# Kernel tuning notes

Hardware: AMD Instinct MI355X
Metric: run time of the kernel (lower is better)

The kernel has to match this reference:

```python
import jax, jax.numpy as jnp
import numpy as np

OBS_LEN = 20
N_COORD = 2
HIDDEN = 1024  # z_dim + c_dim = 512 + 512
N = 4096


def setup_inputs() -> dict:
    key = jax.random.key(0)
    ks = jax.random.split(key, 6)
    obs_traj_rel = jax.random.normal(ks[0], (OBS_LEN, N, N_COORD), dtype=jnp.float32)
    pred_lstm_hidden = jax.random.normal(ks[1], (N, HIDDEN), dtype=jnp.float32)
    # LSTMCell params (PyTorch layout): weight_ih [4H, in], weight_hh [4H, H],
    # initialized N(0, 0.1); biases zero (per _initialize_weights).
    W_ih = 0.1 * jax.random.normal(ks[2], (4 * HIDDEN, N_COORD), dtype=jnp.float32)
    W_hh = 0.1 * jax.random.normal(ks[3], (4 * HIDDEN, HIDDEN), dtype=jnp.float32)
    b_ih = jnp.zeros((4 * HIDDEN,), dtype=jnp.float32)
    b_hh = jnp.zeros((4 * HIDDEN,), dtype=jnp.float32)
    # hidden2pos Linear: weight [n_coord, H], bias zero
    W_out = 0.1 * jax.random.normal(ks[4], (N_COORD, HIDDEN), dtype=jnp.float32)
    b_out = jnp.zeros((N_COORD,), dtype=jnp.float32)
    return {
        "obs_traj_rel": obs_traj_rel,
        "pred_lstm_hidden": pred_lstm_hidden,
        "W_ih": W_ih,
        "W_hh": W_hh,
        "b_ih": b_ih,
        "b_hh": b_hh,
        "W_out": W_out,
        "b_out": b_out,
        "variant_feats": 1,
    }


def reference(obs_traj_rel, pred_lstm_hidden, W_ih, W_hh, b_ih, b_hh, W_out, b_out, variant_feats):
    # Step 0 consumes obs[0]; step i>=1 consumes obs[i-1] (per the original loop).
    x_seq = jnp.concatenate([obs_traj_rel[:1], obs_traj_rel[:-1]], axis=0)[..., :N_COORD]
    c0 = jnp.zeros_like(pred_lstm_hidden)

    def step(carry, x_t):
        h, c = carry
        # PyTorch LSTMCell: gates = x W_ih^T + b_ih + h W_hh^T + b_hh, order i,f,g,o
        gates = x_t @ W_ih.T + b_ih + h @ W_hh.T + b_hh
        i, f, g, o = jnp.split(gates, 4, axis=-1)
        c = jax.nn.sigmoid(f) * c + jax.nn.sigmoid(i) * jnp.tanh(g)
        h = jax.nn.sigmoid(o) * jnp.tanh(c)
        out = h @ W_out.T + b_out  # [N, n_coord]
        return (h, c), out

    _, outs = jax.lax.scan(step, (pred_lstm_hidden, c0), x_seq)
    return outs  # [obs_len, N, n_coord]
```

## Files before the change

kernel.cpp:

```cpp
#include <hip/hip_runtime.h>
#include <hip/hip_bf16.h>
#include <stdint.h>

#define N_BATCH 4096
#define HID     1024
#define OBSLEN  20

#define BM  256
#define BK  64

using short8 = __attribute__((ext_vector_type(8))) short;
using f32x4  = __attribute__((ext_vector_type(4))) float;

#define AS1 __attribute__((address_space(1)))
#define AS3 __attribute__((address_space(3)))

__device__ __forceinline__ float rcpf(float x) { return __builtin_amdgcn_rcpf(x); }
__device__ __forceinline__ float sigf(float x) { return rcpf(1.f + __expf(-x)); }
__device__ __forceinline__ float tanh_(float x) {
    float a = fminf(15.f, fmaxf(-15.f, x));
    float t = __expf(-2.f * a);
    return (1.f - t) * rcpf(1.f + t);
}
__device__ __forceinline__ unsigned short f2bf(float f) {
    __hip_bfloat16 b = __float2bfloat16(f);
    return *reinterpret_cast<unsigned short*>(&b);
}
__device__ __forceinline__ float bf2f(unsigned short u) {
    unsigned int x = ((unsigned int)u) << 16;
    return __uint_as_float(x);
}

__global__ __launch_bounds__(256) void prep_kernel(
    const float4* __restrict__ Whh, const float4* __restrict__ h0,
    ushort4* __restrict__ Wg, ushort4* __restrict__ hb, float4* __restrict__ c, int n4)
{
    int i = blockIdx.x * 256 + threadIdx.x;
    if (i < n4) {
        float4 h = h0[i];
        hb[i] = make_ushort4(f2bf(h.x), f2bf(h.y), f2bf(h.z), f2bf(h.w));
        c[i] = make_float4(0.f, 0.f, 0.f, 0.f);
        int R  = i >> 8, k4 = i & 255;
        int by = R >> 8, cp = R & 255;
        int g  = (cp >> 4) & 3;
        int hl = ((cp >> 6) << 4) | (cp & 15);
        int orig = g * HID + by * 64 + hl;
        float4 w = Whh[orig * 256 + k4];
        Wg[i] = make_ushort4(f2bf(w.x), f2bf(w.y), f2bf(w.z), f2bf(w.w));
    }
}

__global__ __launch_bounds__(512, 2) void lstm_step_kernel(
    const ushort* __restrict__ hin,
    const ushort* __restrict__ Wg,
    const float*  __restrict__ xt,
    const float*  __restrict__ Wih,
    const float*  __restrict__ bih,
    const float*  __restrict__ bhh,
    float*        __restrict__ cst,
    ushort*       __restrict__ hout)
{
    __shared__ __align__(16) char lds[131072];
    const int tid  = threadIdx.x;
    const int lane = tid & 63, l15 = lane & 15, l4 = lane >> 4;
    const int wid  = tid >> 6, wr = wid >> 2, wc = wid & 3;

    const int L    = blockIdx.x + (int)gridDim.x * blockIdx.y;
    const int xcd  = L & 7, slot = L >> 3;
    const int xb   = slot & 15;
    const int yb   = (xcd << 1) | (slot >> 4);
    const int m0   = xb * BM;
    const int by   = yb;
    const int bid  = yb * 16 + xb;

    const int rowS = tid >> 3;
    const int offS = ((tid & 7) * 16) ^ ((rowS & 7) << 4);
    const ushort* aS = hin + (size_t)(m0 + rowS) * HID + (offS >> 1);
    const ushort* bS = Wg  + (size_t)(by * 256 + rowS) * HID + (offS >> 1);
    char* aD = lds + tid * 16;
    char* bD = lds + 65536 + tid * 16;

    auto stA = [&](int s, int k0, int r) {
        __builtin_amdgcn_global_load_lds(
            (const AS1 void*)(aS + k0 + (size_t)r * 64 * HID),
            (AS3 void*)(aD + s * 32768 + r * 8192), 16, 0, 0);
    };
    auto stB = [&](int s, int k0, int r) {
        __builtin_amdgcn_global_load_lds(
            (const AS1 void*)(bS + k0 + (size_t)r * 64 * HID),
            (AS3 void*)(bD + s * 32768 + r * 8192), 16, 0, 0);
    };

    const int swz = (l15 & 7) << 4;
    const int kb0 = (l4 * 16) ^ swz;
    const int aRd = (wr * 128 + l15) * 128 + kb0;
    const int bRd = 65536 + (wc * 64 + l15) * 128 + kb0;

    f32x4 acc[8][4];
#pragma unroll
    for (int f = 0; f < 8; ++f)
#pragma unroll
        for (int n = 0; n < 4; ++n)
            acc[f][n] = (f32x4){0.f, 0.f, 0.f, 0.f};

    short8 af_cur[4], af_nxt[4], bf_cur[4], bf_nxt[4];

#pragma unroll
    for (int r = 0; r < 4; ++r) stA(0, 0, r);
#pragma unroll
    for (int r = 0; r < 4; ++r) stB(0, 0, r);
#pragma unroll
    for (int r = 0; r < 4; ++r) stA(1, 64, r);
    __syncthreads();
#pragma unroll
    for (int f = 0; f < 4; ++f) af_cur[f] = *(const short8*)(lds + aRd + f * 2048);
#pragma unroll
    for (int n = 0; n < 4; ++n) bf_cur[n] = *(const short8*)(lds + bRd + n * 2048);

    const int NK = HID / BK;
    for (int kt = 0; kt < NK; ++kt) {
        const int s = kt & 1, s1 = s ^ 1;
        const int aB = s * 32768 + aRd;
        const int bB = s * 32768 + bRd;

        if (kt < NK - 1) {
#pragma unroll
            for (int r = 0; r < 4; ++r) stB(s1, (kt + 1) * BK, r);
        }
#pragma unroll
        for (int f = 0; f < 4; ++f) af_nxt[f] = *(const short8*)(lds + aB + (f + 4) * 2048);
#pragma unroll
        for (int n = 0; n < 4; ++n) bf_nxt[n] = *(const short8*)(lds + ((bB + n * 2048) ^ 64));
        __builtin_amdgcn_s_setprio(1);
#pragma unroll
        for (int f = 0; f < 4; ++f)
#pragma unroll
            for (int n = 0; n < 4; ++n)
                acc[f][n] = __builtin_amdgcn_mfma_f32_16x16x32_bf16(af_cur[f], bf_cur[n], acc[f][n], 0, 0, 0);
        __builtin_amdgcn_s_setprio(0);

#pragma unroll
        for (int f = 0; f < 4; ++f) af_cur[f] = *(const short8*)(lds + ((aB + f * 2048) ^ 64));
        __builtin_amdgcn_s_setprio(1);
#pragma unroll
        for (int f = 0; f < 4; ++f)
#pragma unroll
            for (int n = 0; n < 4; ++n)
                acc[f + 4][n] = __builtin_amdgcn_mfma_f32_16x16x32_bf16(af_nxt[f], bf_cur[n], acc[f + 4][n], 0, 0, 0);
        __builtin_amdgcn_s_setprio(0);

#pragma unroll
        for (int f = 0; f < 4; ++f) af_nxt[f] = *(const short8*)(lds + ((aB + (f + 4) * 2048) ^ 64));
        __builtin_amdgcn_s_setprio(1);
#pragma unroll
        for (int f = 0; f < 4; ++f)
#pragma unroll
            for (int n = 0; n < 4; ++n)
                acc[f][n] = __builtin_amdgcn_mfma_f32_16x16x32_bf16(af_cur[f], bf_nxt[n], acc[f][n], 0, 0, 0);
        __builtin_amdgcn_s_setprio(0);
        __syncthreads();

        if (kt < NK - 2) {
#pragma unroll
            for (int r = 0; r < 4; ++r) stA(s, (kt + 2) * BK, r);
        }
        if (kt < NK - 1) {
#pragma unroll
            for (int f = 0; f < 4; ++f) af_cur[f] = *(const short8*)(lds + s1 * 32768 + aRd + f * 2048);
#pragma unroll
            for (int n = 0; n < 4; ++n) bf_cur[n] = *(const short8*)(lds + s1 * 32768 + bRd + n * 2048);
        }
        __builtin_amdgcn_s_setprio(1);
#pragma unroll
        for (int f = 0; f < 4; ++f)
#pragma unroll
            for (int n = 0; n < 4; ++n)
                acc[f + 4][n] = __builtin_amdgcn_mfma_f32_16x16x32_bf16(af_nxt[f], bf_nxt[n], acc[f + 4][n], 0, 0, 0);
        __builtin_amdgcn_s_setprio(0);
    }

    float4* c4 = (float4*)cst + (size_t)bid * 4096;
    float4 cv[8];
#pragma unroll
    for (int f = 0; f < 8; ++f) cv[f] = c4[f * 512 + tid];

    const int hcg = by * 64 + wc * 16 + l15;
    float wi0[4], wi1[4], bs_[4];
#pragma unroll
    for (int n = 0; n < 4; ++n) {
        int j = n * HID + hcg;
        wi0[n] = Wih[j * 2 + 0];
        wi1[n] = Wih[j * 2 + 1];
        bs_[n] = bih[j] + bhh[j];
    }
    const float2* xt2 = (const float2*)xt;
#pragma unroll
    for (int f = 0; f < 8; ++f) {
#pragma unroll
        for (int r = 0; r < 4; ++r) {
            int nrow = m0 + wr * 128 + f * 16 + l4 * 4 + r;
            float2 x = xt2[nrow];
            float gi = acc[f][0][r] + x.x * wi0[0] + x.y * wi1[0] + bs_[0];
            float gf = acc[f][1][r] + x.x * wi0[1] + x.y * wi1[1] + bs_[1];
            float gg = acc[f][2][r] + x.x * wi0[2] + x.y * wi1[2] + bs_[2];
            float go = acc[f][3][r] + x.x * wi0[3] + x.y * wi1[3] + bs_[3];
            float iv = sigf(gi), fv = sigf(gf);
            float gv = tanh_(gg), ov = sigf(go);
            float cn = fv * cv[f][r] + iv * gv;
            cv[f][r] = cn;
            hout[(size_t)nrow * HID + hcg] = f2bf(ov * tanh_(cn));
        }
        c4[f * 512 + tid] = cv[f];
    }
}

__global__ __launch_bounds__(256) void out_proj_kernel(
    const ushort* __restrict__ h, const float* __restrict__ Wout,
    const float* __restrict__ bout, float* __restrict__ outt)
{
    const int wid = threadIdx.x >> 6, lane = threadIdx.x & 63;
    const int row = blockIdx.x * 4 + wid;
    const ushort* hr = h + (size_t)row * HID + lane * 16;
    float a0 = 0.f, a1 = 0.f;
#pragma unroll
    for (int half = 0; half < 2; ++half) {
        short8 hv = *(const short8*)(hr + half * 8);
#pragma unroll
        for (int j = 0; j < 8; ++j) {
            int k = lane * 16 + half * 8 + j;
            float f = bf2f((unsigned short)hv[j]);
            a0 += f * Wout[k];
            a1 += f * Wout[HID + k];
        }
    }
#pragma unroll
    for (int off = 32; off > 0; off >>= 1) {
        a0 += __shfl_down(a0, off);
        a1 += __shfl_down(a1, off);
    }
    if (lane == 0) {
        outt[row * 2 + 0] = a0 + bout[0];
        outt[row * 2 + 1] = a1 + bout[1];
    }
}

extern "C" void kernel_launch(void* const* d_in, const int* in_sizes, int n_in,
                              void* d_out, int out_size, void* d_ws, size_t ws_size,
                              hipStream_t stream) {
    const float* obs  = (const float*)d_in[0];
    const float* h0   = (const float*)d_in[1];
    const float* Wih  = (const float*)d_in[2];
    const float* Whh  = (const float*)d_in[3];
    const float* bih  = (const float*)d_in[4];
    const float* bhh  = (const float*)d_in[5];
    const float* Wout = (const float*)d_in[6];
    const float* bout = (const float*)d_in[7];
    float* out = (float*)d_out;

    char* ws = (char*)d_ws;
    ushort* Wg = (ushort*)(ws);
    ushort* hA = (ushort*)(ws + (8  << 20));
    ushort* hB = (ushort*)(ws + (16 << 20));
    float*  c  = (float* )(ws + (24 << 20));

    prep_kernel<<<4096, 256, 0, stream>>>((const float4*)Whh, (const float4*)h0,
                                          (ushort4*)Wg, (ushort4*)hA, (float4*)c,
                                          N_BATCH * HID / 4);

    ushort* hin = hA;
    ushort* hou = hB;
    for (int t = 0; t < OBSLEN; ++t) {
        const float* xt = obs + (size_t)(t == 0 ? 0 : (t - 1)) * N_BATCH * 2;
        lstm_step_kernel<<<dim3(N_BATCH / BM, (4 * HID) / 256), 512, 0, stream>>>(
            hin, Wg, xt, Wih, bih, bhh, c, hou);
        out_proj_kernel<<<N_BATCH / 4, 256, 0, stream>>>(
            hou, Wout, bout, out + (size_t)t * N_BATCH * 2);
        ushort* tmp = hin; hin = hou; hou = tmp;
    }
}
```

Before: 868.9 us.

## Use 4-wave blocks with 128x128 per-wave tiles and explicit waitcnt pipelining

```diff
diff --git a/kernel.cpp b/kernel.cpp
--- a/kernel.cpp
+++ b/kernel.cpp
@@ -50,7 +50,7 @@
     }
 }
 
-__global__ __launch_bounds__(512, 2) void lstm_step_kernel(
+__global__ __launch_bounds__(256, 1) void lstm_step_kernel(
     const ushort* __restrict__ hin,
     const ushort* __restrict__ Wg,
     const float*  __restrict__ xt,
@@ -63,7 +63,7 @@
     __shared__ __align__(16) char lds[131072];
     const int tid  = threadIdx.x;
     const int lane = tid & 63, l15 = lane & 15, l4 = lane >> 4;
-    const int wid  = tid >> 6, wr = wid >> 2, wc = wid & 3;
+    const int wid  = tid >> 6, wr = wid >> 1, wcn = wid & 1;
 
     const int L    = blockIdx.x + (int)gridDim.x * blockIdx.y;
     const int xcd  = L & 7, slot = L >> 3;
@@ -82,40 +82,41 @@
 
     auto stA = [&](int s, int k0, int r) {
         __builtin_amdgcn_global_load_lds(
-            (const AS1 void*)(aS + k0 + (size_t)r * 64 * HID),
-            (AS3 void*)(aD + s * 32768 + r * 8192), 16, 0, 0);
+            (const AS1 void*)(aS + k0 + (size_t)r * 32 * HID),
+            (AS3 void*)(aD + s * 32768 + r * 4096), 16, 0, 0);
     };
     auto stB = [&](int s, int k0, int r) {
         __builtin_amdgcn_global_load_lds(
-            (const AS1 void*)(bS + k0 + (size_t)r * 64 * HID),
-            (AS3 void*)(bD + s * 32768 + r * 8192), 16, 0, 0);
+            (const AS1 void*)(bS + k0 + (size_t)r * 32 * HID),
+            (AS3 void*)(bD + s * 32768 + r * 4096), 16, 0, 0);
     };
 
     const int swz = (l15 & 7) << 4;
     const int kb0 = (l4 * 16) ^ swz;
     const int aRd = (wr * 128 + l15) * 128 + kb0;
-    const int bRd = 65536 + (wc * 64 + l15) * 128 + kb0;
-
-    f32x4 acc[8][4];
+    const int bRd = 65536 + (wcn * 128 + l15) * 128 + kb0;
+
+    f32x4 acc[8][8];
 #pragma unroll
     for (int f = 0; f < 8; ++f)
 #pragma unroll
-        for (int n = 0; n < 4; ++n)
+        for (int n = 0; n < 8; ++n)
             acc[f][n] = (f32x4){0.f, 0.f, 0.f, 0.f};
 
-    short8 af_cur[4], af_nxt[4], bf_cur[4], bf_nxt[4];
-
-#pragma unroll
-    for (int r = 0; r < 4; ++r) stA(0, 0, r);
-#pragma unroll
-    for (int r = 0; r < 4; ++r) stB(0, 0, r);
-#pragma unroll
-    for (int r = 0; r < 4; ++r) stA(1, 64, r);
-    __syncthreads();
-#pragma unroll
-    for (int f = 0; f < 4; ++f) af_cur[f] = *(const short8*)(lds + aRd + f * 2048);
-#pragma unroll
-    for (int n = 0; n < 4; ++n) bf_cur[n] = *(const short8*)(lds + bRd + n * 2048);
+    short8 af[8], bf[8], af2[8], bf2[8];
+
+#pragma unroll
+    for (int r = 0; r < 8; ++r) stA(0, 0, r);
+#pragma unroll
+    for (int r = 0; r < 8; ++r) stB(0, 0, r);
+#pragma unroll
+    for (int r = 0; r < 8; ++r) stA(1, 64, r);
+    asm volatile("s_waitcnt vmcnt(8)" ::: "memory");
+    __builtin_amdgcn_s_barrier();
+#pragma unroll
+    for (int f = 0; f < 8; ++f) af[f] = *(const short8*)(lds + aRd + f * 2048);
+#pragma unroll
+    for (int n = 0; n < 8; ++n) bf[n] = *(const short8*)(lds + bRd + n * 2048);
 
     const int NK = HID / BK;
     for (int kt = 0; kt < NK; ++kt) {
@@ -125,92 +126,80 @@
 
         if (kt < NK - 1) {
 #pragma unroll
-            for (int r = 0; r < 4; ++r) stB(s1, (kt + 1) * BK, r);
-        }
-#pragma unroll
-        for (int f = 0; f < 4; ++f) af_nxt[f] = *(const short8*)(lds + aB + (f + 4) * 2048);
-#pragma unroll
-        for (int n = 0; n < 4; ++n) bf_nxt[n] = *(const short8*)(lds + ((bB + n * 2048) ^ 64));
-        __builtin_amdgcn_s_setprio(1);
-#pragma unroll
-        for (int f = 0; f < 4; ++f)
-#pragma unroll
-            for (int n = 0; n < 4; ++n)
-                acc[f][n] = __builtin_amdgcn_mfma_f32_16x16x32_bf16(af_cur[f], bf_cur[n], acc[f][n], 0, 0, 0);
-        __builtin_amdgcn_s_setprio(0);
-
-#pragma unroll
-        for (int f = 0; f < 4; ++f) af_cur[f] = *(const short8*)(lds + ((aB + f * 2048) ^ 64));
-        __builtin_amdgcn_s_setprio(1);
-#pragma unroll
-        for (int f = 0; f < 4; ++f)
-#pragma unroll
-            for (int n = 0; n < 4; ++n)
-                acc[f + 4][n] = __builtin_amdgcn_mfma_f32_16x16x32_bf16(af_nxt[f], bf_cur[n], acc[f + 4][n], 0, 0, 0);
-        __builtin_amdgcn_s_setprio(0);
-
-#pragma unroll
-        for (int f = 0; f < 4; ++f) af_nxt[f] = *(const short8*)(lds + ((aB + (f + 4) * 2048) ^ 64));
-        __builtin_amdgcn_s_setprio(1);
-#pragma unroll
-        for (int f = 0; f < 4; ++f)
-#pragma unroll
-            for (int n = 0; n < 4; ++n)
-                acc[f][n] = __builtin_amdgcn_mfma_f32_16x16x32_bf16(af_cur[f], bf_nxt[n], acc[f][n], 0, 0, 0);
-        __builtin_amdgcn_s_setprio(0);
-        __syncthreads();
+            for (int r = 0; r < 8; ++r) stB(s1, (kt + 1) * BK, r);
+        }
+#pragma unroll
+        for (int f = 0; f < 8; ++f) af2[f] = *(const short8*)(lds + ((aB + f * 2048) ^ 64));
+#pragma unroll
+        for (int n = 0; n < 8; ++n) bf2[n] = *(const short8*)(lds + ((bB + n * 2048) ^ 64));
+#pragma unroll
+        for (int f = 0; f < 8; ++f)
+#pragma unroll
+            for (int n = 0; n < 8; ++n)
+                acc[f][n] = __builtin_amdgcn_mfma_f32_16x16x32_bf16(af[f], bf[n], acc[f][n], 0, 0, 0);
+
+        __builtin_amdgcn_sched_barrier(0);
+        asm volatile("s_waitcnt lgkmcnt(0)" ::: "memory");
+        __builtin_amdgcn_s_barrier();
+        __builtin_amdgcn_sched_barrier(0);
 
         if (kt < NK - 2) {
 #pragma unroll
-            for (int r = 0; r < 4; ++r) stA(s, (kt + 2) * BK, r);
+            for (int r = 0; r < 8; ++r) stA(s, (kt + 2) * BK, r);
         }
         if (kt < NK - 1) {
-#pragma unroll
-            for (int f = 0; f < 4; ++f) af_cur[f] = *(const short8*)(lds + s1 * 32768 + aRd + f * 2048);
-#pragma unroll
-            for (int n = 0; n < 4; ++n) bf_cur[n] = *(const short8*)(lds + s1 * 32768 + bRd + n * 2048);
-        }
-        __builtin_amdgcn_s_setprio(1);
-#pragma unroll
-        for (int f = 0; f < 4; ++f)
-#pragma unroll
-            for (int n = 0; n < 4; ++n)
-                acc[f + 4][n] = __builtin_amdgcn_mfma_f32_16x16x32_bf16(af_nxt[f], bf_nxt[n], acc[f + 4][n], 0, 0, 0);
-        __builtin_amdgcn_s_setprio(0);
+            if (kt < NK - 2) asm volatile("s_waitcnt vmcnt(8)" ::: "memory");
+            else             asm volatile("s_waitcnt vmcnt(0)" ::: "memory");
+            __builtin_amdgcn_sched_barrier(0);
+#pragma unroll
+            for (int f = 0; f < 8; ++f) af[f] = *(const short8*)(lds + s1 * 32768 + aRd + f * 2048);
+#pragma unroll
+            for (int n = 0; n < 8; ++n) bf[n] = *(const short8*)(lds + s1 * 32768 + bRd + n * 2048);
+        }
+#pragma unroll
+        for (int f = 0; f < 8; ++f)
+#pragma unroll
+            for (int n = 0; n < 8; ++n)
+                acc[f][n] = __builtin_amdgcn_mfma_f32_16x16x32_bf16(af2[f], bf2[n], acc[f][n], 0, 0, 0);
     }
 
     float4* c4 = (float4*)cst + (size_t)bid * 4096;
-    float4 cv[8];
-#pragma unroll
-    for (int f = 0; f < 8; ++f) cv[f] = c4[f * 512 + tid];
-
-    const int hcg = by * 64 + wc * 16 + l15;
-    float wi0[4], wi1[4], bs_[4];
-#pragma unroll
-    for (int n = 0; n < 4; ++n) {
-        int j = n * HID + hcg;
-        wi0[n] = Wih[j * 2 + 0];
-        wi1[n] = Wih[j * 2 + 1];
-        bs_[n] = bih[j] + bhh[j];
-    }
     const float2* xt2 = (const float2*)xt;
+
+    float wi0[2][4], wi1[2][4], bs_[2][4];
+#pragma unroll
+    for (int hb = 0; hb < 2; ++hb) {
+        const int hcg = by * 64 + (wcn * 2 + hb) * 16 + l15;
+#pragma unroll
+        for (int g = 0; g < 4; ++g) {
+            int j = g * HID + hcg;
+            wi0[hb][g] = Wih[j * 2 + 0];
+            wi1[hb][g] = Wih[j * 2 + 1];
+            bs_[hb][g] = bih[j] + bhh[j];
+        }
+    }
 #pragma unroll
     for (int f = 0; f < 8; ++f) {
 #pragma unroll
-        for (int r = 0; r < 4; ++r) {
-            int nrow = m0 + wr * 128 + f * 16 + l4 * 4 + r;
-            float2 x = xt2[nrow];
-            float gi = acc[f][0][r] + x.x * wi0[0] + x.y * wi1[0] + bs_[0];
-            float gf = acc[f][1][r] + x.x * wi0[1] + x.y * wi1[1] + bs_[1];
-            float gg = acc[f][2][r] + x.x * wi0[2] + x.y * wi1[2] + bs_[2];
-            float go = acc[f][3][r] + x.x * wi0[3] + x.y * wi1[3] + bs_[3];
-            float iv = sigf(gi), fv = sigf(gf);
-            float gv = tanh_(gg), ov = sigf(go);
-            float cn = fv * cv[f][r] + iv * gv;
-            cv[f][r] = cn;
-            hout[(size_t)nrow * HID + hcg] = f2bf(ov * tanh_(cn));
-        }
-        c4[f * 512 + tid] = cv[f];
+        for (int hb = 0; hb < 2; ++hb) {
+            const int hcg = by * 64 + (wcn * 2 + hb) * 16 + l15;
+            float4 cv = c4[(f * 2 + hb) * 256 + tid];
+#pragma unroll
+            for (int r = 0; r < 4; ++r) {
+                int nrow = m0 + wr * 128 + f * 16 + l4 * 4 + r;
+                float2 x = xt2[nrow];
+                float gi = acc[f][hb * 4 + 0][r] + x.x * wi0[hb][0] + x.y * wi1[hb][0] + bs_[hb][0];
+                float gf = acc[f][hb * 4 + 1][r] + x.x * wi0[hb][1] + x.y * wi1[hb][1] + bs_[hb][1];
+                float gg = acc[f][hb * 4 + 2][r] + x.x * wi0[hb][2] + x.y * wi1[hb][2] + bs_[hb][2];
+                float go = acc[f][hb * 4 + 3][r] + x.x * wi0[hb][3] + x.y * wi1[hb][3] + bs_[hb][3];
+                float iv = sigf(gi), fv = sigf(gf);
+                float gv = tanh_(gg), ov = sigf(go);
+                float cn = fv * cv[r] + iv * gv;
+                cv[r] = cn;
+                hout[(size_t)nrow * HID + hcg] = f2bf(ov * tanh_(cn));
+            }
+            c4[(f * 2 + hb) * 256 + tid] = cv;
+        }
     }
 }
 
@@ -271,7 +260,7 @@
     ushort* hou = hB;
     for (int t = 0; t < OBSLEN; ++t) {
         const float* xt = obs + (size_t)(t == 0 ? 0 : (t - 1)) * N_BATCH * 2;
-        lstm_step_kernel<<<dim3(N_BATCH / BM, (4 * HID) / 256), 512, 0, stream>>>(
+        lstm_step_kernel<<<dim3(N_BATCH / BM, (4 * HID) / 256), 256, 0, stream>>>(
             hin, Wg, xt, Wih, bih, bhh, c, hou);
         out_proj_kernel<<<N_BATCH / 4, 256, 0, stream>>>(
             hou, Wout, bout, out + (size_t)t * N_BATCH * 2);
```

After: 1.259 ms. 1.45x slower.
